# Kernel tuning notes

Hardware: AMD Instinct MI355X
Metric: run time of the kernel (lower is better)

The kernel has to match this reference:

```python
import jax, jax.numpy as jnp
from jax import lax
import numpy as np

EPS = 1e-5

def _bn(x, g, b, m, v):
    # inference-mode BatchNorm2d over channel dim (NCHW)
    scale = (g * lax.rsqrt(v + EPS))[None, :, None, None]
    return (x - m[None, :, None, None]) * scale + b[None, :, None, None]

def _conv(x, w, dil, pad):
    return lax.conv_general_dilated(
        x, w, window_strides=(1, 1), padding=[(pad, pad), (pad, pad)],
        rhs_dilation=(dil, dil), dimension_numbers=('NCHW', 'OIHW', 'NCHW'))

def _interleave(b0, b1, b2, b3):
    # out[2i+r, 2j+c] = branch[2r+c][i, j]  (equivalent to the mask*nearest-upsample trick)
    bs, C, H, W = b0.shape
    row0 = jnp.stack([b0, b1], axis=-1)          # (bs,C,H,W,2) -> c
    row1 = jnp.stack([b2, b3], axis=-1)
    s = jnp.stack([row0, row1], axis=-2)          # (bs,C,H,W,2,2) -> (...,r,c)
    return s.transpose(0, 1, 2, 4, 3, 5).reshape(bs, C, 2 * H, 2 * W)

def setup_inputs() -> dict:
    key = jax.random.key(0)
    ks = iter(jax.random.split(key, 40))
    B, Cin, Cout, H = 8, 256, 128, 64
    inp = {"x": jax.random.normal(next(ks), (B, Cin, H, H), jnp.float32)}
    inp["w0"] = jax.random.normal(next(ks), (Cout, Cin, 1, 1), jnp.float32) * 0.05
    for i in (1, 2, 3):
        inp[f"w{i}"] = jax.random.normal(next(ks), (Cout, Cin, 3, 3), jnp.float32) * 0.02
    inp["wp"] = jax.random.normal(next(ks), (Cout, Cout, 1, 1), jnp.float32) * 0.05
    for t in ("0", "1", "2", "3", "p"):
        inp[f"g{t}"] = 1.0 + 0.1 * jax.random.normal(next(ks), (Cout,), jnp.float32)
        inp[f"b{t}"] = 0.1 * jax.random.normal(next(ks), (Cout,), jnp.float32)
        inp[f"m{t}"] = 0.05 * jax.random.normal(next(ks), (Cout,), jnp.float32)
        inp[f"v{t}"] = jax.random.uniform(next(ks), (Cout,), jnp.float32, 0.5, 1.5)
    return inp

def reference(x, w0, w1, w2, w3, wp,
              g0, b0, m0, v0, g1, b1, m1, v1,
              g2, b2, m2, v2, g3, b3, m3, v3,
              gp, bp, mp, vp):
    RATES = (6, 12, 18)
    br0 = jax.nn.relu(_bn(_conv(x, w0, 1, 0), g0, b0, m0, v0))
    br1 = jax.nn.relu(_bn(_conv(x, w1, RATES[0], RATES[0]), g1, b1, m1, v1))
    br2 = jax.nn.relu(_bn(_conv(x, w2, RATES[1], RATES[1]), g2, b2, m2, v2))
    br3 = jax.nn.relu(_bn(_conv(x, w3, RATES[2], RATES[2]), g3, b3, m3, v3))
    up = _interleave(br0, br1, br2, br3)          # (B, Cout, 2H, 2W)
    return jax.nn.relu(_bn(_conv(up, wp, 1, 0), gp, bp, mp, vp))  # dropout: eval identity
```

## Files before the change

### kernel.cpp

```cpp
#include <hip/hip_runtime.h>
#include <stdint.h>

typedef unsigned int uint32;
typedef uint16_t u16;
typedef short short8 __attribute__((ext_vector_type(8)));
typedef short shortx4 __attribute__((ext_vector_type(4)));
typedef float floatx4 __attribute__((ext_vector_type(4)));

#define BN_EPS 1e-5f

#define OFF0 0
#define OFF1 32768
#define OFF2 327680
#define OFF3 622592
#define OFFP 917504
#define WPK_SHORTS 933888
#define U_B0 4096
#define U_B  36864
#define U_TOT 116736

__device__ __forceinline__ u16 f2bf(float f) {
  uint32 u = __float_as_uint(f);
  u += 0x7fffu + ((u >> 16) & 1u);
  return (u16)(u >> 16);
}

__global__ void k_xcvt(const float* __restrict__ x, u16* __restrict__ xb, int n8) {
  int i = blockIdx.x * 256 + threadIdx.x;
  if (i >= n8) return;
  const floatx4* p = (const floatx4*)(x + (size_t)i * 8);
  floatx4 a = p[0], b = p[1];
  union { short8 s; u16 us[8]; } o;
  o.us[0]=f2bf(a[0]); o.us[1]=f2bf(a[1]); o.us[2]=f2bf(a[2]); o.us[3]=f2bf(a[3]);
  o.us[4]=f2bf(b[0]); o.us[5]=f2bf(b[1]); o.us[6]=f2bf(b[2]); o.us[7]=f2bf(b[3]);
  ((short8*)xb)[i] = o.s;
}

__global__ void k_wpack(const float* __restrict__ w0, const float* __restrict__ w1,
                        const float* __restrict__ w2, const float* __restrict__ w3,
                        const float* __restrict__ wp, u16* __restrict__ wpk) {
  int g = blockIdx.x * 256 + threadIdx.x;
  if (g >= U_TOT) return;
  const float* w; int Cin, t, q, u, off; bool k3;
  if (g < U_B0) {
    int blk = g >> 10; w = w0; Cin = 256; k3 = false; t = 0; q = blk; u = g & 1023;
    off = OFF0 + blk * 8192;
  } else if (g < U_B0 + U_B) {
    int g1 = g - U_B0; int blk = g1 >> 10; w = w1; Cin = 256; k3 = true;
    t = blk >> 2; q = blk & 3; u = g1 & 1023; off = OFF1 + blk * 8192;
  } else if (g < U_B0 + 2*U_B) {
    int g1 = g - (U_B0 + U_B); int blk = g1 >> 10; w = w2; Cin = 256; k3 = true;
    t = blk >> 2; q = blk & 3; u = g1 & 1023; off = OFF2 + blk * 8192;
  } else if (g < U_B0 + 3*U_B) {
    int g1 = g - (U_B0 + 2*U_B); int blk = g1 >> 10; w = w3; Cin = 256; k3 = true;
    t = blk >> 2; q = blk & 3; u = g1 & 1023; off = OFF3 + blk * 8192;
  } else {
    int g1 = g - (U_B0 + 3*U_B); int blk = g1 >> 10; w = wp; Cin = 128; k3 = false;
    t = 0; q = blk; u = g1 & 1023; off = OFFP + blk * 8192;
  }
  int co = u >> 3, slot = u & 7;
  int sl = slot ^ (co & 7);
  int ci0 = q * 64 + sl * 8;
  int kh = k3 ? (t / 3) : 0, kw = k3 ? (t % 3) : 0;
  union { short8 s; u16 us[8]; } v;
  #pragma unroll
  for (int e = 0; e < 8; ++e) {
    int ci = ci0 + e;
    float wv = k3 ? w[((co * Cin + ci) * 3 + kh) * 3 + kw] : w[co * Cin + ci];
    v.us[e] = f2bf(wv);
  }
  *(short8*)(wpk + off + u * 8) = v.s;
}

__global__ void k_bn(const float* g0,const float* b0,const float* m0,const float* v0,
                     const float* g1,const float* b1,const float* m1,const float* v1,
                     const float* g2,const float* b2,const float* m2,const float* v2,
                     const float* g3,const float* b3,const float* m3,const float* v3,
                     const float* gp,const float* bp,const float* mp,const float* vp,
                     float* __restrict__ bn) {
  int i = blockIdx.x * 256 + threadIdx.x;
  if (i >= 640) return;
  int t = i >> 7, co = i & 127;
  const float *G, *B, *M, *V;
  if      (t == 0) { G=g0; B=b0; M=m0; V=v0; }
  else if (t == 1) { G=g1; B=b1; M=m1; V=v1; }
  else if (t == 2) { G=g2; B=b2; M=m2; V=v2; }
  else if (t == 3) { G=g3; B=b3; M=m3; V=v3; }
  else             { G=gp; B=bp; M=mp; V=vp; }
  float s = G[co] * rsqrtf(V[co] + BN_EPS);
  bn[t * 256 + co]       = s;
  bn[t * 256 + 128 + co] = B[co] - M[co] * s;
}

__global__ __launch_bounds__(256, 3)
void k_main(const u16* __restrict__ xb, const u16* __restrict__ wpk,
            const float* __restrict__ bn, float* __restrict__ out) {
  __shared__ __align__(16) u16 As[8192];
  __shared__ __align__(16) u16 BP[16384];

  int tid = threadIdx.x;
  int bid = blockIdx.x;
  int n = bid & 7;
  int rest = bid >> 3;
  int b = rest & 3;
  int tile = rest >> 2;
  int i0 = tile * 2;
  int lane = tid & 63, wid = tid >> 6;
  int wm = wid >> 1, wn = wid & 1;
  int m16 = lane & 15, hh = lane >> 4;

  const u16* xg = xb + (size_t)n * (256 * 4096);
  int d = (b == 0) ? 0 : ((b == 1) ? 6 : ((b == 2) ? 12 : 18));
  int NS = ((b == 0) ? 1 : 9) * 4;
  int woff8 = ((b == 0) ? OFF0 : (b == 1) ? OFF1 : (b == 2) ? OFF2 : OFF3) / 8;

  const short8* wpk8 = (const short8*)wpk;
  short8* AsS8 = (short8*)As;
  short8* BsS8 = (short8*)BP;
  const short8* PsS8 = (const short8*)BP;

  floatx4 acc[4][4];
  #pragma unroll
  for (int a1 = 0; a1 < 4; ++a1)
    #pragma unroll
    for (int a2 = 0; a2 < 4; ++a2) acc[a1][a2] = (floatx4){0.f, 0.f, 0.f, 0.f};

  short8 ra[4];
  uint32 rbv[16];
  bool inb0 = false, inb1 = false;

  auto prefetch = [&](int s) {
    int abase = woff8 + s * 1024;
    #pragma unroll
    for (int w = 0; w < 4; ++w) ra[w] = wpk8[abase + w * 256 + tid];
    int t = s >> 2, q = s & 3;
    int di = d * (t / 3 - 1);
    int dj = d * (t % 3 - 1);
    #pragma unroll
    for (int pu = 0; pu < 2; ++pu) {
      int pidx = pu * 256 + tid;
      int cg = pidx >> 6;
      int pp = pidx & 63;
      int row = pp >> 5;
      int col0 = (pp & 31) * 2;
      int ii = i0 + row + di;
      int jj = col0 + dj;
      bool inb = (ii >= 0) && (ii < 64) && (jj >= 0) && (jj < 64);
      if (pu == 0) inb0 = inb; else inb1 = inb;
      size_t offs = inb ? ((size_t)(q * 64 + cg * 8) * 4096 + (ii * 64 + jj)) : 0;
      const u16* src = xg + offs;
      #pragma unroll
      for (int e = 0; e < 8; ++e)
        rbv[pu * 8 + e] = *(const uint32*)(src + (size_t)e * 4096);
    }
  };

  prefetch(0);

  for (int s = 0; s < NS; ++s) {
    __builtin_amdgcn_s_barrier();
    #pragma unroll
    for (int w = 0; w < 4; ++w) AsS8[w * 256 + tid] = ra[w];
    #pragma unroll
    for (int pu = 0; pu < 2; ++pu) {
      bool inb = (pu == 0) ? inb0 : inb1;
      int pidx = pu * 256 + tid;
      int cg = pidx >> 6;
      int pp = pidx & 63;
      int row = pp >> 5;
      int col0 = (pp & 31) * 2;
      int px0 = row * 64 + col0;
      union { short8 s; u16 us[8]; } lo, hi;
      #pragma unroll
      for (int e = 0; e < 8; ++e) {
        uint32 vv = inb ? rbv[pu * 8 + e] : 0u;
        lo.us[e] = (u16)(vv & 0xffffu);
        hi.us[e] = (u16)(vv >> 16);
      }
      int sw = (px0 >> 1) & 7;
      BsS8[px0 * 8 + (cg ^ sw)] = lo.s;
      BsS8[(px0 + 1) * 8 + (cg ^ sw)] = hi.s;
    }
    if (s + 1 < NS) prefetch(s + 1);
    asm volatile("s_waitcnt lgkmcnt(0)" ::: "memory");
    __builtin_amdgcn_s_barrier();
    __builtin_amdgcn_sched_barrier(0);
    #pragma unroll
    for (int kk = 0; kk < 2; ++kk) {
      short8 af[4], bfr[4];
      #pragma unroll
      for (int f = 0; f < 4; ++f) {
        int row = wm * 64 + f * 16 + m16;
        af[f] = AsS8[row * 8 + ((kk * 4 + hh) ^ (row & 7))];
      }
      #pragma unroll
      for (int f = 0; f < 4; ++f) {
        int px = wn * 64 + f * 16 + m16;
        bfr[f] = BsS8[px * 8 + ((kk * 4 + hh) ^ ((px >> 1) & 7))];
      }
      #pragma unroll
      for (int fm = 0; fm < 4; ++fm)
        #pragma unroll
        for (int fn = 0; fn < 4; ++fn)
          acc[fm][fn] = __builtin_amdgcn_mfma_f32_16x16x32_bf16(
              af[fm], bfr[fn], acc[fm][fn], 0, 0, 0);
    }
  }

  __syncthreads();
  #pragma unroll
  for (int fm = 0; fm < 4; ++fm) {
    int co_base = wm * 64 + fm * 16 + hh * 4;
    float sc[4], sh[4];
    #pragma unroll
    for (int r = 0; r < 4; ++r) {
      sc[r] = bn[b * 256 + co_base + r];
      sh[r] = bn[b * 256 + 128 + co_base + r];
    }
    #pragma unroll
    for (int fn = 0; fn < 4; ++fn) {
      int px = wn * 64 + fn * 16 + m16;
      int sw = (px >> 1) & 7;
      int slot = (co_base >> 3) ^ sw;
      union { shortx4 s4; u16 us[4]; } pk;
      #pragma unroll
      for (int r = 0; r < 4; ++r)
        pk.us[r] = f2bf(fmaxf(acc[fm][fn][r] * sc[r] + sh[r], 0.f));
      *(shortx4*)&BP[px * 128 + slot * 8 + (co_base & 7)] = pk.s4;
    }
  }

  floatx4 acc2[4][4];
  #pragma unroll
  for (int a1 = 0; a1 < 4; ++a1)
    #pragma unroll
    for (int a2 = 0; a2 < 4; ++a2) acc2[a1][a2] = (floatx4){0.f, 0.f, 0.f, 0.f};

  for (int q = 0; q < 2; ++q) {
    if (q == 1) __syncthreads();
    int abase = OFFP / 8 + q * 1024;
    #pragma unroll
    for (int w = 0; w < 4; ++w) AsS8[w * 256 + tid] = wpk8[abase + w * 256 + tid];
    __syncthreads();
    #pragma unroll
    for (int kk = 0; kk < 2; ++kk) {
      short8 af[4], bfr[4];
      #pragma unroll
      for (int f = 0; f < 4; ++f) {
        int row = wm * 64 + f * 16 + m16;
        af[f] = AsS8[row * 8 + ((kk * 4 + hh) ^ (row & 7))];
      }
      #pragma unroll
      for (int f = 0; f < 4; ++f) {
        int px = wn * 64 + f * 16 + m16;
        int slot = q * 8 + kk * 4 + hh;
        bfr[f] = PsS8[px * 16 + (slot ^ ((px >> 1) & 7))];
      }
      #pragma unroll
      for (int fm = 0; fm < 4; ++fm)
        #pragma unroll
        for (int fn = 0; fn < 4; ++fn)
          acc2[fm][fn] = __builtin_amdgcn_mfma_f32_16x16x32_bf16(
              af[fm], bfr[fn], acc2[fm][fn], 0, 0, 0);
    }
  }

  int rb2 = b >> 1, cb = b & 1;
  #pragma unroll
  for (int fm = 0; fm < 4; ++fm) {
    #pragma unroll
    for (int r = 0; r < 4; ++r) {
      int co = wm * 64 + fm * 16 + hh * 4 + r;
      float s  = bn[1024 + co];
      float sh = bn[1024 + 128 + co];
      #pragma unroll
      for (int fn = 0; fn < 4; ++fn) {
        int px = wn * 64 + fn * 16 + m16;
        int i = i0 + (px >> 6), j = px & 63;
        float v = fmaxf(acc2[fm][fn][r] * s + sh, 0.f);
        out[(((n * 128 + co) * 128) + (2 * i + rb2)) * 128 + (2 * j + cb)] = v;
      }
    }
  }
}

extern "C" void kernel_launch(void* const* d_in, const int* in_sizes, int n_in,
                              void* d_out, int out_size, void* d_ws, size_t ws_size,
                              hipStream_t stream) {
  const float* x  = (const float*)d_in[0];
  const float* w0 = (const float*)d_in[1];
  const float* w1 = (const float*)d_in[2];
  const float* w2 = (const float*)d_in[3];
  const float* w3 = (const float*)d_in[4];
  const float* wp = (const float*)d_in[5];

  u16* xbuf = (u16*)d_ws;
  u16* wpk  = (u16*)d_ws + 8388608;
  float* bn = (float*)((char*)d_ws + 16777216 + 1867776);

  k_xcvt<<<4096, 256, 0, stream>>>(x, xbuf, 1048576);
  k_wpack<<<456, 256, 0, stream>>>(w0, w1, w2, w3, wp, wpk);
  k_bn<<<3, 256, 0, stream>>>(
      (const float*)d_in[6],  (const float*)d_in[7],  (const float*)d_in[8],  (const float*)d_in[9],
      (const float*)d_in[10], (const float*)d_in[11], (const float*)d_in[12], (const float*)d_in[13],
      (const float*)d_in[14], (const float*)d_in[15], (const float*)d_in[16], (const float*)d_in[17],
      (const float*)d_in[18], (const float*)d_in[19], (const float*)d_in[20], (const float*)d_in[21],
      (const float*)d_in[22], (const float*)d_in[23], (const float*)d_in[24], (const float*)d_in[25],
      bn);
  k_main<<<1024, 256, 0, stream>>>(xbuf, wpk, bn, (float*)d_out);
}
```

Measured before the change: 121.0 us.

## Convert input to padded channel-last bf16 layout for vectorized halo-free loads

The conversion kernel now writes x as a per-row, channel-innermost (NHWC-like) bf16 buffer with 18 zero columns of padding on each side, plus a shared zero row for out-of-range rows. The main kernel then loads 16-byte short8 vectors straight into shared memory, with no per-element bounds checks or 16-bit unpacking, and a simpler LDS swizzle. It also remaps the branch index per block to spread the uneven branch work across the grid. The cost is a larger workspace and a conversion pass that is strided on reads and writes padding.

```diff
diff --git a/kernel.cpp b/kernel.cpp
--- a/kernel.cpp
+++ b/kernel.cpp
@@ -8,6 +8,11 @@
 typedef float floatx4 __attribute__((ext_vector_type(4)));
 
 #define BN_EPS 1e-5f
+
+#define XROW 25600
+#define XPLANE 1638400
+#define XB_SHORTS 13107200
+#define ZROW_SHORTS 25600
 
 #define OFF0 0
 #define OFF1 32768
@@ -25,15 +30,32 @@
   return (u16)(u >> 16);
 }
 
-__global__ void k_xcvt(const float* __restrict__ x, u16* __restrict__ xb, int n8) {
-  int i = blockIdx.x * 256 + threadIdx.x;
-  if (i >= n8) return;
-  const floatx4* p = (const floatx4*)(x + (size_t)i * 8);
-  floatx4 a = p[0], b = p[1];
-  union { short8 s; u16 us[8]; } o;
-  o.us[0]=f2bf(a[0]); o.us[1]=f2bf(a[1]); o.us[2]=f2bf(a[2]); o.us[3]=f2bf(a[3]);
-  o.us[4]=f2bf(b[0]); o.us[5]=f2bf(b[1]); o.us[6]=f2bf(b[2]); o.us[7]=f2bf(b[3]);
-  ((short8*)xb)[i] = o.s;
+__global__ void k_xcvt(const float* __restrict__ x, u16* __restrict__ xb) {
+  int bid = blockIdx.x, tid = threadIdx.x;
+  if (bid == 512) {
+    uint32* z = (uint32*)(xb + XB_SHORTS);
+    #pragma unroll
+    for (int r = 0; r < 50; ++r) z[r * 256 + tid] = 0;
+    return;
+  }
+  int n = bid >> 6, i = bid & 63;
+  uint32* rw = (uint32*)(xb + (size_t)n * XPLANE + (size_t)i * XROW);
+  #pragma unroll
+  for (int e = 0; e < 18; ++e) {
+    int idx = e * 256 + tid;
+    int colid = idx >> 7;
+    int jp = (colid < 18) ? colid : (colid + 64);
+    rw[jp * 128 + (idx & 127)] = 0;
+  }
+  int ci2 = tid & 127, jh = tid >> 7;
+  const float* xs = x + ((size_t)(n * 256 + 2 * ci2) * 64 + i) * 64 + jh * 32;
+  #pragma unroll 4
+  for (int j = 0; j < 32; ++j) {
+    float f0 = xs[j];
+    float f1 = xs[4096 + j];
+    uint32 pk = (uint32)f2bf(f0) | ((uint32)f2bf(f1) << 16);
+    rw[(jh * 32 + j + 18) * 128 + ci2] = pk;
+  }
 }
 
 __global__ void k_wpack(const float* __restrict__ w0, const float* __restrict__ w1,
@@ -102,14 +124,15 @@
   int bid = blockIdx.x;
   int n = bid & 7;
   int rest = bid >> 3;
-  int b = rest & 3;
   int tile = rest >> 2;
+  int b = (rest ^ (rest >> 5)) & 3;
   int i0 = tile * 2;
   int lane = tid & 63, wid = tid >> 6;
   int wm = wid >> 1, wn = wid & 1;
   int m16 = lane & 15, hh = lane >> 4;
 
-  const u16* xg = xb + (size_t)n * (256 * 4096);
+  const u16* xg = xb + (size_t)n * XPLANE;
+  const u16* zr = xb + XB_SHORTS;
   int d = (b == 0) ? 0 : ((b == 1) ? 6 : ((b == 2) ? 12 : 18));
   int NS = ((b == 0) ? 1 : 9) * 4;
   int woff8 = ((b == 0) ? OFF0 : (b == 1) ? OFF1 : (b == 2) ? OFF2 : OFF3) / 8;
@@ -126,8 +149,8 @@
     for (int a2 = 0; a2 < 4; ++a2) acc[a1][a2] = (floatx4){0.f, 0.f, 0.f, 0.f};
 
   short8 ra[4];
-  uint32 rbv[16];
-  bool inb0 = false, inb1 = false;
+  short8 rb[4];
+  int cg = tid & 7, pxo = tid >> 3;
 
   auto prefetch = [&](int s) {
     int abase = woff8 + s * 1024;
@@ -137,21 +160,12 @@
     int di = d * (t / 3 - 1);
     int dj = d * (t % 3 - 1);
     #pragma unroll
-    for (int pu = 0; pu < 2; ++pu) {
-      int pidx = pu * 256 + tid;
-      int cg = pidx >> 6;
-      int pp = pidx & 63;
-      int row = pp >> 5;
-      int col0 = (pp & 31) * 2;
-      int ii = i0 + row + di;
-      int jj = col0 + dj;
-      bool inb = (ii >= 0) && (ii < 64) && (jj >= 0) && (jj < 64);
-      if (pu == 0) inb0 = inb; else inb1 = inb;
-      size_t offs = inb ? ((size_t)(q * 64 + cg * 8) * 4096 + (ii * 64 + jj)) : 0;
-      const u16* src = xg + offs;
-      #pragma unroll
-      for (int e = 0; e < 8; ++e)
-        rbv[pu * 8 + e] = *(const uint32*)(src + (size_t)e * 4096);
+    for (int k = 0; k < 4; ++k) {
+      int px = k * 32 + pxo;
+      int ii = i0 + (k >> 1) + di;
+      const u16* base = (ii >= 0 && ii < 64) ? (xg + ii * XROW) : zr;
+      int jj = (px & 63) + 18 + dj;
+      rb[k] = *(const short8*)(base + jj * 256 + q * 64 + cg * 8);
     }
   };
 
@@ -162,24 +176,9 @@
     #pragma unroll
     for (int w = 0; w < 4; ++w) AsS8[w * 256 + tid] = ra[w];
     #pragma unroll
-    for (int pu = 0; pu < 2; ++pu) {
-      bool inb = (pu == 0) ? inb0 : inb1;
-      int pidx = pu * 256 + tid;
-      int cg = pidx >> 6;
-      int pp = pidx & 63;
-      int row = pp >> 5;
-      int col0 = (pp & 31) * 2;
-      int px0 = row * 64 + col0;
-      union { short8 s; u16 us[8]; } lo, hi;
-      #pragma unroll
-      for (int e = 0; e < 8; ++e) {
-        uint32 vv = inb ? rbv[pu * 8 + e] : 0u;
-        lo.us[e] = (u16)(vv & 0xffffu);
-        hi.us[e] = (u16)(vv >> 16);
-      }
-      int sw = (px0 >> 1) & 7;
-      BsS8[px0 * 8 + (cg ^ sw)] = lo.s;
-      BsS8[(px0 + 1) * 8 + (cg ^ sw)] = hi.s;
+    for (int k = 0; k < 4; ++k) {
+      int px = k * 32 + pxo;
+      BsS8[px * 8 + (cg ^ (px & 7))] = rb[k];
     }
     if (s + 1 < NS) prefetch(s + 1);
     asm volatile("s_waitcnt lgkmcnt(0)" ::: "memory");
@@ -196,7 +195,7 @@
       #pragma unroll
       for (int f = 0; f < 4; ++f) {
         int px = wn * 64 + f * 16 + m16;
-        bfr[f] = BsS8[px * 8 + ((kk * 4 + hh) ^ ((px >> 1) & 7))];
+        bfr[f] = BsS8[px * 8 + ((kk * 4 + hh) ^ (px & 7))];
       }
       #pragma unroll
       for (int fm = 0; fm < 4; ++fm)
@@ -295,10 +294,10 @@
   const float* wp = (const float*)d_in[5];
 
   u16* xbuf = (u16*)d_ws;
-  u16* wpk  = (u16*)d_ws + 8388608;
-  float* bn = (float*)((char*)d_ws + 16777216 + 1867776);
-
-  k_xcvt<<<4096, 256, 0, stream>>>(x, xbuf, 1048576);
+  u16* wpk  = (u16*)d_ws + (XB_SHORTS + ZROW_SHORTS);
+  float* bn = (float*)((char*)d_ws + (size_t)(XB_SHORTS + ZROW_SHORTS + WPK_SHORTS) * 2);
+
+  k_xcvt<<<513, 256, 0, stream>>>(x, xbuf);
   k_wpack<<<456, 256, 0, stream>>>(w0, w1, w2, w3, wp, wpk);
   k_bn<<<3, 256, 0, stream>>>(
       (const float*)d_in[6],  (const float*)d_in[7],  (const float*)d_in[8],  (const float*)d_in[9],
```

Result: faster. 109.2 us (-9.7%).
